# Kernel tuning notes

Measured on AMD Instinct MI355X. Metric: run time of the kernel, lower is better.

## Reference

```python
import jax, jax.numpy as jnp
import numpy as np

P = 7          # output_size
SCALE = 0.125  # spatial_scale
S = 2          # sampling_ratio


def setup_inputs() -> dict:
    key = jax.random.key(0)
    k1, k2, k3, k4, k5, k6 = jax.random.split(key, 6)
    N, C, H, W, R = 8, 256, 100, 100, 512
    x = jax.random.normal(k1, (N, C, H, W), dtype=jnp.float32)
    b = jax.random.randint(k2, (R,), 0, N).astype(jnp.float32)
    x1 = jax.random.uniform(k3, (R,)) * 600.0
    y1 = jax.random.uniform(k4, (R,)) * 600.0
    bw = 10.0 + jax.random.uniform(k5, (R,)) * 190.0
    bh = 10.0 + jax.random.uniform(k6, (R,)) * 190.0
    rois = jnp.stack([b, x1, y1, x1 + bw, y1 + bh], axis=1).astype(jnp.float32)
    return {"x": x, "rois": rois}


def _axis_terms(c, L):
    # Per-axis bilinear terms, matching torchvision bilinear_interpolate.
    valid = (c > -1.0) & (c < L)          # whole sample zeroed if out of range
    c = jnp.clip(c, 0.0, L - 1.0)          # low clamp at 0; >=L-1 -> frac 0
    lo = jnp.minimum(jnp.floor(c).astype(jnp.int32), L - 1)
    hi = jnp.minimum(lo + 1, L - 1)
    frac = c - lo.astype(c.dtype)
    w_lo = jnp.where(valid, 1.0 - frac, 0.0)
    w_hi = jnp.where(valid, frac, 0.0)
    return lo, hi, w_lo, w_hi


def roi_align(x, rois):
    # aligned=True RoIAlign. x: [N,C,H,W], rois: [R,5] -> [R,C,P,P]
    N, C, H, W = x.shape
    b = rois[:, 0].astype(jnp.int32)
    sx = rois[:, 1] * SCALE - 0.5
    sy = rois[:, 2] * SCALE - 0.5
    bin_w = (rois[:, 3] * SCALE - 0.5 - sx) / P
    bin_h = (rois[:, 4] * SCALE - 0.5 - sy) / P

    frac = (jnp.arange(S, dtype=x.dtype) + 0.5) / S   # sample offset within bin
    bins = jnp.arange(P, dtype=x.dtype)
    grid = bins[None, :, None] + frac[None, None, :]   # [1,P,S]
    ys = sy[:, None, None] + grid * bin_h[:, None, None]  # [R,P,S]
    xs = sx[:, None, None] + grid * bin_w[:, None, None]  # [R,P,S]

    yl, yh, wy1, wy2 = _axis_terms(ys, H)
    xl, xh, wx1, wx2 = _axis_terms(xs, W)

    bb = b[:, None, None, None, None]
    Yl, Yh = yl[:, :, :, None, None], yh[:, :, :, None, None]  # [R,P,S,1,1]
    Xl, Xh = xl[:, None, None, :, :], xh[:, None, None, :, :]  # [R,1,1,P,S]

    def g(Y, X):
        # gather -> [R,Py,Sy,Px,Sx,C]
        return x[bb, :, Y, X]

    def w(wy, wx):
        return (wy[:, :, :, None, None] * wx[:, None, None, :, :])[..., None]

    val = (g(Yl, Xl) * w(wy1, wx1) + g(Yl, Xh) * w(wy1, wx2)
           + g(Yh, Xl) * w(wy2, wx1) + g(Yh, Xh) * w(wy2, wx2))
    # average over the SxS sampling grid per bin
    out = val.sum(axis=(2, 4)) / float(S * S)   # [R,Py,Px,C]
    return jnp.transpose(out, (0, 3, 1, 2))      # [R,C,P,P]


def reference(x, rois):
    return roi_align(x, rois)
```

## Files before the change

kernel.cpp:

```cpp
#include <hip/hip_runtime.h>

#define POOL 7
#define CCH 256
#define GCH 4
#define HH 100
#define WW 100
#define HW (HH * WW)
#define MAXTH 28
#define NTAP 14
#define RECI 128
#define NT 256

static constexpr float SCALE = 0.125f;

__device__ __attribute__((aligned(16))) int g_rec[1024 * RECI];

__device__ __forceinline__ void tap_calc(float s0, float step, int k, int L,
                                         int& lo, int& hi, float& w1, float& w2)
{
    const int   p  = k >> 1, si = k & 1;
    const float g  = (float)p + ((float)si + 0.5f) * 0.5f;
    const float c  = s0 + g * step;
    const float Lf = (float)L;
    const bool  valid = (c > -1.0f) && (c < Lf);
    float cl = fminf(fmaxf(c, 0.0f), Lf - 1.0f);
    lo = (int)floorf(cl);
    if (lo > L - 1) lo = L - 1;
    hi = lo + 1;
    if (hi > L - 1) hi = L - 1;
    const float fr = cl - (float)lo;
    w1 = valid ? 1.0f - fr : 0.0f;
    w2 = valid ? fr : 0.0f;
}

__global__ __launch_bounds__(64) void roi_pre(const float* __restrict__ rois,
                                              int* __restrict__ rec, int R)
{
    const int r = blockIdx.x;
    if (r >= R) return;
    int* rr = (rec ? rec : g_rec) + r * RECI;
    const int t = threadIdx.x;

    const float sx0 = rois[r * 5 + 1] * SCALE - 0.5f;
    const float sy0 = rois[r * 5 + 2] * SCALE - 0.5f;
    const float bw  = (rois[r * 5 + 3] * SCALE - 0.5f - sx0) * (1.0f / POOL);
    const float bh  = (rois[r * 5 + 4] * SCALE - 0.5f - sy0) * (1.0f / POOL);

    if (t < 2 * NTAP) {
        const int   axis = (t >= NTAP) ? 1 : 0;
        const int   k    = axis ? t - NTAP : t;
        const float s0   = axis ? sy0 : sx0;
        const float st   = axis ? bh : bw;
        const int   L    = axis ? HH : WW;
        int lo, hi, lo0, u0; float w1, w2, ua, ub;
        tap_calc(s0, st, k, L, lo, hi, w1, w2);
        tap_calc(s0, st, 0, L, lo0, u0, ua, ub);
        const int base = axis ? lo0 : (lo0 & ~3);
        int* tp = rr + 8 + (axis ? 4 * NTAP : 0) + k * 4;
        tp[0] = max(lo - base, 0);
        tp[1] = max(hi - base, 0);
        tp[2] = __float_as_int(w1);
        tp[3] = __float_as_int(w2);
    } else if (t == 2 * NTAP) {
        int xl0, xh0, xl13, xh13, yl0, yh0, yl13, yh13; float a, b;
        tap_calc(sx0, bw, 0,        WW, xl0,  xh0,  a, b);
        tap_calc(sx0, bw, NTAP - 1, WW, xl13, xh13, a, b);
        tap_calc(sy0, bh, 0,        HH, yl0,  yh0,  a, b);
        tap_calc(sy0, bh, NTAP - 1, HH, yl13, yh13, a, b);
        const int xmin_al = xl0 & ~3;
        int TH  = yh13 - yl0 + 1; if (TH > MAXTH) TH = MAXTH;
        int nb4 = (xh13 - xmin_al) / 4 + 1;
        if (nb4 > 8) nb4 = 8;
        rr[0] = (int)rois[r * 5 + 0];
        rr[1] = xmin_al;
        rr[2] = yl0;
        rr[3] = TH;
        rr[4] = nb4;
        rr[5] = (65536 + nb4 - 1) / nb4;
    }
}

__global__ __launch_bounds__(NT, 8) void roi_main(
    const float* __restrict__ x, const int* __restrict__ rec_in,
    float* __restrict__ out)
{
    __shared__ float tile[GCH * MAXTH * 32];

    const int bid  = blockIdx.x;
    const int r    = bid >> 6;
    const int c0   = (bid & 63) * GCH;
    const int t    = threadIdx.x;
    const int ch   = t >> 6;
    const int lane = t & 63;

    const int* rr = (rec_in ? rec_in : g_rec) + r * RECI;
    const int n       = rr[0];
    const int xmin_al = rr[1];
    const int ymin    = rr[2];
    const int TH      = rr[3];
    const int nb4     = rr[4];
    const int magic   = rr[5];

    const int bin = (lane < POOL * POOL) ? lane : POOL * POOL - 1;
    const int py  = bin / POOL;
    const int px  = bin - py * POOL;
    const int4* tp = (const int4*)(rr + 8);
    const int4 xt0 = tp[px * 2],        xt1 = tp[px * 2 + 1];
    const int4 yt0 = tp[NTAP + py * 2], yt1 = tp[NTAP + py * 2 + 1];

    const int chstride = TH * (nb4 << 2);
    const int tot      = TH * nb4;

    {
        const float* xb = x + ((size_t)(n * CCH + c0 + ch)) * HW
                            + (size_t)ymin * WW + xmin_al;
        float* lbase = tile + ch * chstride;
        for (int idx = lane; idx < tot; idx += 64) {
            const int row = (idx * magic) >> 16;
            const int b   = idx - row * nb4;
            __builtin_amdgcn_global_load_lds(
                (const __attribute__((address_space(1))) void*)(xb + row * WW + (b << 2)),
                (__attribute__((address_space(3))) void*)(lbase + (idx << 2)),
                16, 0, 0);
        }
    }
    asm volatile("s_waitcnt vmcnt(0)" ::: "memory");

    if (lane < POOL * POOL) {
        const int   TWp = nb4 << 2;
        const float* tc = tile + ch * chstride;
        const int   rl0 = yt0.x * TWp, rh0 = yt0.y * TWp;
        const int   rl1 = yt1.x * TWp, rh1 = yt1.y * TWp;
        const float wy10 = __int_as_float(yt0.z), wy20 = __int_as_float(yt0.w);
        const float wy11 = __int_as_float(yt1.z), wy21 = __int_as_float(yt1.w);
        const float wx10 = __int_as_float(xt0.z), wx20 = __int_as_float(xt0.w);
        const float wx11 = __int_as_float(xt1.z), wx21 = __int_as_float(xt1.w);

        float acc;
        acc  = wy10 * (wx10 * tc[rl0 + xt0.x] + wx20 * tc[rl0 + xt0.y])
             + wy20 * (wx10 * tc[rh0 + xt0.x] + wx20 * tc[rh0 + xt0.y]);
        acc += wy10 * (wx11 * tc[rl0 + xt1.x] + wx21 * tc[rl0 + xt1.y])
             + wy20 * (wx11 * tc[rh0 + xt1.x] + wx21 * tc[rh0 + xt1.y]);
        acc += wy11 * (wx10 * tc[rl1 + xt0.x] + wx20 * tc[rl1 + xt0.y])
             + wy21 * (wx10 * tc[rh1 + xt0.x] + wx20 * tc[rh1 + xt0.y]);
        acc += wy11 * (wx11 * tc[rl1 + xt1.x] + wx21 * tc[rl1 + xt1.y])
             + wy21 * (wx11 * tc[rh1 + xt1.x] + wx21 * tc[rh1 + xt1.y]);

        out[(size_t)(r * CCH + c0 + ch) * (POOL * POOL) + bin] = acc * 0.25f;
    }
}

extern "C" void kernel_launch(void* const* d_in, const int* in_sizes, int n_in,
                              void* d_out, int out_size, void* d_ws, size_t ws_size,
                              hipStream_t stream) {
    const float* x    = (const float*)d_in[0];
    const float* rois = (const float*)d_in[1];
    float*       out  = (float*)d_out;

    const int R = in_sizes[1] / 5;
    int* rec = (ws_size >= (size_t)R * RECI * sizeof(int)) ? (int*)d_ws : nullptr;

    roi_pre<<<R, 64, 0, stream>>>(rois, rec, R);
    roi_main<<<R * (CCH / GCH), NT, 0, stream>>>(x, rec, out);
}
```

Measured before the change: 42.42 us.

## Process two channels per wave with unrolled async tile loads and split waits

Each 64-lane wave now handles two channels instead of one, so each block covers 8 channels and half as many blocks are launched. The tile load loop is specialised by load count through a template switch, fully unrolled, and issues loads for both channels together. Bilinear offsets and weights are computed while the loads are in flight, and the first channel is reduced after a partial vmcnt wait. This cuts per-block setup and lets address math overlap memory latency, but raises LDS per block, drops the occupancy hint, and the partial wait gives little real overlap.

```diff
diff --git a/kernel.cpp b/kernel.cpp
--- a/kernel.cpp
+++ b/kernel.cpp
@@ -2,7 +2,6 @@
 
 #define POOL 7
 #define CCH 256
-#define GCH 4
 #define HH 100
 #define WW 100
 #define HW (HH * WW)
@@ -10,6 +9,8 @@
 #define NTAP 14
 #define RECI 128
 #define NT 256
+#define ITEMS 2
+#define SLOTF 896
 
 static constexpr float SCALE = 0.125f;
 
@@ -80,73 +81,130 @@
     }
 }
 
-__global__ __launch_bounds__(NT, 8) void roi_main(
-    const float* __restrict__ x, const int* __restrict__ rec_in,
-    float* __restrict__ out)
-{
-    __shared__ float tile[GCH * MAXTH * 32];
-
-    const int bid  = blockIdx.x;
-    const int r    = bid >> 6;
-    const int c0   = (bid & 63) * GCH;
-    const int t    = threadIdx.x;
-    const int ch   = t >> 6;
-    const int lane = t & 63;
-
-    const int* rr = (rec_in ? rec_in : g_rec) + r * RECI;
-    const int n       = rr[0];
-    const int xmin_al = rr[1];
-    const int ymin    = rr[2];
-    const int TH      = rr[3];
-    const int nb4     = rr[4];
-    const int magic   = rr[5];
-
+template <int NJ>
+__device__ __forceinline__ void run2(
+    const float* __restrict__ x, float* __restrict__ out,
+    float* slot, const int* __restrict__ rr,
+    int n, int c0, int r, int xmin_al, int ymin,
+    int TWp, int tot, int magic, int nb4, int lane)
+{
     const int bin = (lane < POOL * POOL) ? lane : POOL * POOL - 1;
     const int py  = bin / POOL;
     const int px  = bin - py * POOL;
     const int4* tp = (const int4*)(rr + 8);
     const int4 xt0 = tp[px * 2],        xt1 = tp[px * 2 + 1];
     const int4 yt0 = tp[NTAP + py * 2], yt1 = tp[NTAP + py * 2 + 1];
-
-    const int chstride = TH * (nb4 << 2);
-    const int tot      = TH * nb4;
-
+    __builtin_amdgcn_sched_barrier(0);
+
+    const float* xa = x + ((size_t)(n * CCH + c0)) * HW
+                        + (size_t)ymin * WW + xmin_al;
+    const float* xb = xa + HW;
+
+    #pragma unroll
+    for (int j = 0; j < NJ; ++j) {
+        const int idx = lane + 64 * j;
+        const int row = (idx * magic) >> 16;
+        const int b   = idx - row * nb4;
+        const int go  = row * WW + (b << 2);
+        float* la = slot + j * 256;
+        float* lb = slot + SLOTF + j * 256;
+        if (j < NJ - 1 || idx < tot) {
+            __builtin_amdgcn_global_load_lds(
+                (const __attribute__((address_space(1))) void*)(xa + go),
+                (__attribute__((address_space(3))) void*)la, 16, 0, 0);
+            __builtin_amdgcn_global_load_lds(
+                (const __attribute__((address_space(1))) void*)(xb + go),
+                (__attribute__((address_space(3))) void*)lb, 16, 0, 0);
+        }
+    }
+
+    int   off[16];
+    float wgt[16];
     {
-        const float* xb = x + ((size_t)(n * CCH + c0 + ch)) * HW
-                            + (size_t)ymin * WW + xmin_al;
-        float* lbase = tile + ch * chstride;
-        for (int idx = lane; idx < tot; idx += 64) {
-            const int row = (idx * magic) >> 16;
-            const int b   = idx - row * nb4;
-            __builtin_amdgcn_global_load_lds(
-                (const __attribute__((address_space(1))) void*)(xb + row * WW + (b << 2)),
-                (__attribute__((address_space(3))) void*)(lbase + (idx << 2)),
-                16, 0, 0);
-        }
-    }
-    asm volatile("s_waitcnt vmcnt(0)" ::: "memory");
-
-    if (lane < POOL * POOL) {
-        const int   TWp = nb4 << 2;
-        const float* tc = tile + ch * chstride;
         const int   rl0 = yt0.x * TWp, rh0 = yt0.y * TWp;
         const int   rl1 = yt1.x * TWp, rh1 = yt1.y * TWp;
         const float wy10 = __int_as_float(yt0.z), wy20 = __int_as_float(yt0.w);
         const float wy11 = __int_as_float(yt1.z), wy21 = __int_as_float(yt1.w);
         const float wx10 = __int_as_float(xt0.z), wx20 = __int_as_float(xt0.w);
         const float wx11 = __int_as_float(xt1.z), wx21 = __int_as_float(xt1.w);
-
-        float acc;
-        acc  = wy10 * (wx10 * tc[rl0 + xt0.x] + wx20 * tc[rl0 + xt0.y])
-             + wy20 * (wx10 * tc[rh0 + xt0.x] + wx20 * tc[rh0 + xt0.y]);
-        acc += wy10 * (wx11 * tc[rl0 + xt1.x] + wx21 * tc[rl0 + xt1.y])
-             + wy20 * (wx11 * tc[rh0 + xt1.x] + wx21 * tc[rh0 + xt1.y]);
-        acc += wy11 * (wx10 * tc[rl1 + xt0.x] + wx20 * tc[rl1 + xt0.y])
-             + wy21 * (wx10 * tc[rh1 + xt0.x] + wx20 * tc[rh1 + xt0.y]);
-        acc += wy11 * (wx11 * tc[rl1 + xt1.x] + wx21 * tc[rl1 + xt1.y])
-             + wy21 * (wx11 * tc[rh1 + xt1.x] + wx21 * tc[rh1 + xt1.y]);
-
-        out[(size_t)(r * CCH + c0 + ch) * (POOL * POOL) + bin] = acc * 0.25f;
+        off[0]  = rl0 + xt0.x;  wgt[0]  = wy10 * wx10;
+        off[1]  = rl0 + xt0.y;  wgt[1]  = wy10 * wx20;
+        off[2]  = rh0 + xt0.x;  wgt[2]  = wy20 * wx10;
+        off[3]  = rh0 + xt0.y;  wgt[3]  = wy20 * wx20;
+        off[4]  = rl0 + xt1.x;  wgt[4]  = wy10 * wx11;
+        off[5]  = rl0 + xt1.y;  wgt[5]  = wy10 * wx21;
+        off[6]  = rh0 + xt1.x;  wgt[6]  = wy20 * wx11;
+        off[7]  = rh0 + xt1.y;  wgt[7]  = wy20 * wx21;
+        off[8]  = rl1 + xt0.x;  wgt[8]  = wy11 * wx10;
+        off[9]  = rl1 + xt0.y;  wgt[9]  = wy11 * wx20;
+        off[10] = rh1 + xt0.x;  wgt[10] = wy21 * wx10;
+        off[11] = rh1 + xt0.y;  wgt[11] = wy21 * wx20;
+        off[12] = rl1 + xt1.x;  wgt[12] = wy11 * wx11;
+        off[13] = rl1 + xt1.y;  wgt[13] = wy11 * wx21;
+        off[14] = rh1 + xt1.x;  wgt[14] = wy21 * wx11;
+        off[15] = rh1 + xt1.y;  wgt[15] = wy21 * wx21;
+    }
+
+    asm volatile("s_waitcnt vmcnt(1)" ::: "memory");
+    float a0 = 0.f, a1 = 0.f, a2 = 0.f, a3 = 0.f;
+    #pragma unroll
+    for (int i = 0; i < 16; i += 4) {
+        a0 += wgt[i + 0] * slot[off[i + 0]];
+        a1 += wgt[i + 1] * slot[off[i + 1]];
+        a2 += wgt[i + 2] * slot[off[i + 2]];
+        a3 += wgt[i + 3] * slot[off[i + 3]];
+    }
+    const float accA = (a0 + a1) + (a2 + a3);
+
+    asm volatile("s_waitcnt vmcnt(0)" ::: "memory");
+    const float* sb = slot + SLOTF;
+    float b0 = 0.f, b1 = 0.f, b2 = 0.f, b3 = 0.f;
+    #pragma unroll
+    for (int i = 0; i < 16; i += 4) {
+        b0 += wgt[i + 0] * sb[off[i + 0]];
+        b1 += wgt[i + 1] * sb[off[i + 1]];
+        b2 += wgt[i + 2] * sb[off[i + 2]];
+        b3 += wgt[i + 3] * sb[off[i + 3]];
+    }
+    const float accB = (b0 + b1) + (b2 + b3);
+
+    if (lane < POOL * POOL) {
+        float* ob = out + ((size_t)(r * CCH + c0)) * (POOL * POOL) + bin;
+        ob[0]           = accA * 0.25f;
+        ob[POOL * POOL] = accB * 0.25f;
+    }
+}
+
+__global__ __launch_bounds__(NT) void roi_main(
+    const float* __restrict__ x, const int* __restrict__ rec_in,
+    float* __restrict__ out)
+{
+    __shared__ float tile[(NT / 64) * ITEMS * SLOTF];
+
+    const int bid  = blockIdx.x;
+    const int r    = bid >> 5;
+    const int g    = bid & 31;
+    const int wid  = threadIdx.x >> 6;
+    const int lane = threadIdx.x & 63;
+    const int c0   = g * (ITEMS * NT / 64) + wid * ITEMS;
+
+    const int* rr = (rec_in ? rec_in : g_rec) + r * RECI;
+    const int4 ra = *(const int4*)rr;
+    const int2 rb = *(const int2*)(rr + 4);
+    const int n = ra.x, xmin_al = ra.y, ymin = ra.z, TH = ra.w;
+    const int nb4 = rb.x, magic = rb.y;
+
+    const int tot = TH * nb4;
+    const int TWp = nb4 << 2;
+    const int nj  = (tot + 63) >> 6;
+
+    float* slot = tile + wid * (ITEMS * SLOTF);
+
+    switch (nj) {
+    case 1:  run2<1>(x, out, slot, rr, n, c0, r, xmin_al, ymin, TWp, tot, magic, nb4, lane); break;
+    case 2:  run2<2>(x, out, slot, rr, n, c0, r, xmin_al, ymin, TWp, tot, magic, nb4, lane); break;
+    case 3:  run2<3>(x, out, slot, rr, n, c0, r, xmin_al, ymin, TWp, tot, magic, nb4, lane); break;
+    default: run2<4>(x, out, slot, rr, n, c0, r, xmin_al, ymin, TWp, tot, magic, nb4, lane); break;
     }
 }
 
@@ -161,5 +219,5 @@
     int* rec = (ws_size >= (size_t)R * RECI * sizeof(int)) ? (int*)d_ws : nullptr;
 
     roi_pre<<<R, 64, 0, stream>>>(rois, rec, R);
-    roi_main<<<R * (CCH / GCH), NT, 0, stream>>>(x, rec, out);
-}
+    roi_main<<<R * 32, NT, 0, stream>>>(x, rec, out);
+}
```

Result: faster. 40.62 us (-4.2%).

## Gather bilinear taps directly from global memory and swizzle block order

Applied to the files above, without the earlier changes.

Removes the shared-memory tile staging (global_load_lds plus waitcnt) and has each lane load its 16 bilinear taps straight from global memory, relying on cache for reuse. Adds a block-index swizzle that spreads consecutive workgroups across the 8 XCDs, so that blocks for the same ROI land on the same XCD's L2. This drops LDS usage and the explicit tile loop, but relies on L2/L1 hits for redundant scattered loads.

```diff
diff --git a/kernel.cpp b/kernel.cpp
--- a/kernel.cpp
+++ b/kernel.cpp
@@ -62,33 +62,28 @@
         tp[2] = __float_as_int(w1);
         tp[3] = __float_as_int(w2);
     } else if (t == 2 * NTAP) {
-        int xl0, xh0, xl13, xh13, yl0, yh0, yl13, yh13; float a, b;
+        int xl0, xh0, yl0, yh0, yl13, yh13; float a, b;
         tap_calc(sx0, bw, 0,        WW, xl0,  xh0,  a, b);
-        tap_calc(sx0, bw, NTAP - 1, WW, xl13, xh13, a, b);
         tap_calc(sy0, bh, 0,        HH, yl0,  yh0,  a, b);
         tap_calc(sy0, bh, NTAP - 1, HH, yl13, yh13, a, b);
         const int xmin_al = xl0 & ~3;
         int TH  = yh13 - yl0 + 1; if (TH > MAXTH) TH = MAXTH;
-        int nb4 = (xh13 - xmin_al) / 4 + 1;
-        if (nb4 > 8) nb4 = 8;
         rr[0] = (int)rois[r * 5 + 0];
         rr[1] = xmin_al;
         rr[2] = yl0;
         rr[3] = TH;
-        rr[4] = nb4;
-        rr[5] = (65536 + nb4 - 1) / nb4;
     }
 }
 
-__global__ __launch_bounds__(NT, 8) void roi_main(
+__global__ __launch_bounds__(NT) void roi_main(
     const float* __restrict__ x, const int* __restrict__ rec_in,
-    float* __restrict__ out)
+    float* __restrict__ out, int nwg)
 {
-    __shared__ float tile[GCH * MAXTH * 32];
-
     const int bid  = blockIdx.x;
-    const int r    = bid >> 6;
-    const int c0   = (bid & 63) * GCH;
+    const int swb  = ((nwg & 7) == 0)
+                   ? ((bid & 7) * (nwg >> 3) + (bid >> 3)) : bid;
+    const int r    = swb >> 6;
+    const int c0   = (swb & 63) * GCH;
     const int t    = threadIdx.x;
     const int ch   = t >> 6;
     const int lane = t & 63;
@@ -97,57 +92,51 @@
     const int n       = rr[0];
     const int xmin_al = rr[1];
     const int ymin    = rr[2];
-    const int TH      = rr[3];
-    const int nb4     = rr[4];
-    const int magic   = rr[5];
 
     const int bin = (lane < POOL * POOL) ? lane : POOL * POOL - 1;
     const int py  = bin / POOL;
     const int px  = bin - py * POOL;
+
     const int4* tp = (const int4*)(rr + 8);
     const int4 xt0 = tp[px * 2],        xt1 = tp[px * 2 + 1];
     const int4 yt0 = tp[NTAP + py * 2], yt1 = tp[NTAP + py * 2 + 1];
 
-    const int chstride = TH * (nb4 << 2);
-    const int tot      = TH * nb4;
+    const float* base = x + ((size_t)(n * CCH + c0 + ch)) * HW
+                          + (size_t)ymin * WW + xmin_al;
 
-    {
-        const float* xb = x + ((size_t)(n * CCH + c0 + ch)) * HW
-                            + (size_t)ymin * WW + xmin_al;
-        float* lbase = tile + ch * chstride;
-        for (int idx = lane; idx < tot; idx += 64) {
-            const int row = (idx * magic) >> 16;
-            const int b   = idx - row * nb4;
-            __builtin_amdgcn_global_load_lds(
-                (const __attribute__((address_space(1))) void*)(xb + row * WW + (b << 2)),
-                (__attribute__((address_space(3))) void*)(lbase + (idx << 2)),
-                16, 0, 0);
-        }
-    }
-    asm volatile("s_waitcnt vmcnt(0)" ::: "memory");
+    const int rl0 = yt0.x * WW, rh0 = yt0.y * WW;
+    const int rl1 = yt1.x * WW, rh1 = yt1.y * WW;
 
-    if (lane < POOL * POOL) {
-        const int   TWp = nb4 << 2;
-        const float* tc = tile + ch * chstride;
-        const int   rl0 = yt0.x * TWp, rh0 = yt0.y * TWp;
-        const int   rl1 = yt1.x * TWp, rh1 = yt1.y * TWp;
-        const float wy10 = __int_as_float(yt0.z), wy20 = __int_as_float(yt0.w);
-        const float wy11 = __int_as_float(yt1.z), wy21 = __int_as_float(yt1.w);
-        const float wx10 = __int_as_float(xt0.z), wx20 = __int_as_float(xt0.w);
-        const float wx11 = __int_as_float(xt1.z), wx21 = __int_as_float(xt1.w);
+    const float v00 = base[rl0 + xt0.x];
+    const float v01 = base[rl0 + xt0.y];
+    const float v02 = base[rh0 + xt0.x];
+    const float v03 = base[rh0 + xt0.y];
+    const float v04 = base[rl0 + xt1.x];
+    const float v05 = base[rl0 + xt1.y];
+    const float v06 = base[rh0 + xt1.x];
+    const float v07 = base[rh0 + xt1.y];
+    const float v08 = base[rl1 + xt0.x];
+    const float v09 = base[rl1 + xt0.y];
+    const float v10 = base[rh1 + xt0.x];
+    const float v11 = base[rh1 + xt0.y];
+    const float v12 = base[rl1 + xt1.x];
+    const float v13 = base[rl1 + xt1.y];
+    const float v14 = base[rh1 + xt1.x];
+    const float v15 = base[rh1 + xt1.y];
 
-        float acc;
-        acc  = wy10 * (wx10 * tc[rl0 + xt0.x] + wx20 * tc[rl0 + xt0.y])
-             + wy20 * (wx10 * tc[rh0 + xt0.x] + wx20 * tc[rh0 + xt0.y]);
-        acc += wy10 * (wx11 * tc[rl0 + xt1.x] + wx21 * tc[rl0 + xt1.y])
-             + wy20 * (wx11 * tc[rh0 + xt1.x] + wx21 * tc[rh0 + xt1.y]);
-        acc += wy11 * (wx10 * tc[rl1 + xt0.x] + wx20 * tc[rl1 + xt0.y])
-             + wy21 * (wx10 * tc[rh1 + xt0.x] + wx20 * tc[rh1 + xt0.y]);
-        acc += wy11 * (wx11 * tc[rl1 + xt1.x] + wx21 * tc[rl1 + xt1.y])
-             + wy21 * (wx11 * tc[rh1 + xt1.x] + wx21 * tc[rh1 + xt1.y]);
+    const float wy10 = __int_as_float(yt0.z), wy20 = __int_as_float(yt0.w);
+    const float wy11 = __int_as_float(yt1.z), wy21 = __int_as_float(yt1.w);
+    const float wx10 = __int_as_float(xt0.z), wx20 = __int_as_float(xt0.w);
+    const float wx11 = __int_as_float(xt1.z), wx21 = __int_as_float(xt1.w);
 
+    float acc;
+    acc  = wy10 * (wx10 * v00 + wx20 * v01) + wy20 * (wx10 * v02 + wx20 * v03);
+    acc += wy10 * (wx11 * v04 + wx21 * v05) + wy20 * (wx11 * v06 + wx21 * v07);
+    acc += wy11 * (wx10 * v08 + wx20 * v09) + wy21 * (wx10 * v10 + wx20 * v11);
+    acc += wy11 * (wx11 * v12 + wx21 * v13) + wy21 * (wx11 * v14 + wx21 * v15);
+
+    if (lane < POOL * POOL)
         out[(size_t)(r * CCH + c0 + ch) * (POOL * POOL) + bin] = acc * 0.25f;
-    }
 }
 
 extern "C" void kernel_launch(void* const* d_in, const int* in_sizes, int n_in,
@@ -160,6 +149,8 @@
     const int R = in_sizes[1] / 5;
     int* rec = (ws_size >= (size_t)R * RECI * sizeof(int)) ? (int*)d_ws : nullptr;
 
+    const int nwg = R * (CCH / GCH);
+
     roi_pre<<<R, 64, 0, stream>>>(rois, rec, R);
-    roi_main<<<R * (CCH / GCH), NT, 0, stream>>>(x, rec, out);
+    roi_main<<<nwg, NT, 0, stream>>>(x, rec, out, nwg);
 }
```

Measured after the change: 100.2 us. +136.3%, slower.
